# Kernel tuning notes

Measured on AMD Instinct MI355X. Metric: run time of the kernel, lower is better.

Reference implementation:

```python
import jax, jax.numpy as jnp
import numpy as np

BS, N, D, H = 4, 2048, 512, 8
DK = D // H
XAVIER_STD = float(np.sqrt(2.0 / (D + D)))  # xavier_normal_, gain=1


def setup_inputs() -> dict:
    key = jax.random.key(0)
    ks = jax.random.split(key, 10)
    Q = jax.random.normal(ks[0], (BS, N, D), jnp.float32)
    K = jax.random.normal(ks[1], (BS, N, D), jnp.float32)
    V = jax.random.normal(ks[2], (BS, N, D), jnp.float32)
    q_mas = jax.random.randint(ks[3], (BS, N, 1), 0, 2).astype(jnp.float32)
    k_mas = jax.random.randint(ks[4], (BS, N, 1), 0, 2).astype(jnp.float32)
    # 0/1 attention mask; force self-edges so no row is fully masked (avoids NaN softmax)
    att_mas = jax.random.randint(ks[5], (BS, N, N), 0, 2).astype(jnp.float32)
    att_mas = jnp.maximum(att_mas, jnp.eye(N, dtype=jnp.float32)[None])
    WQ = jax.random.normal(ks[6], (D, D), jnp.float32) * XAVIER_STD
    WK = jax.random.normal(ks[7], (D, D), jnp.float32) * XAVIER_STD
    WV = jax.random.normal(ks[8], (D, D), jnp.float32) * XAVIER_STD
    WO = jax.random.normal(ks[9], (D, D), jnp.float32) * XAVIER_STD
    return {"Q": Q, "K": K, "V": V, "q_mas": q_mas, "k_mas": k_mas,
            "att_mas": att_mas, "WQ": WQ, "WK": WK, "WV": WV, "WO": WO}


def reference(Q, K, V, q_mas, k_mas, att_mas, WQ, WK, WV, WO):
    bs, n, d = Q.shape
    h, dk = H, DK
    qm = q_mas.reshape(bs, 1, n, 1)  # (bs,1,n,1)
    km = k_mas.reshape(bs, 1, n, 1)
    # nn.Linear (no bias): x @ W.T ; split heads -> (bs,h,n,dk); apply pre-masks
    Qh = qm * (Q @ WQ.T).reshape(bs, n, h, dk).transpose(0, 2, 1, 3)
    Kh = km * (K @ WK.T).reshape(bs, n, h, dk).transpose(0, 2, 1, 3)
    Vh = km * (V @ WV.T).reshape(bs, n, h, dk).transpose(0, 2, 1, 3)
    scores = jnp.einsum('bhqd,bhkd->bhqk', Qh, Kh) / jnp.sqrt(jnp.float32(dk))
    mas = att_mas.reshape(bs, 1, n, n)
    scores = jnp.where(mas.astype(bool), scores, -jnp.inf)
    attn = jax.nn.softmax(scores, axis=-1) * mas
    y = jnp.einsum('bhqk,bhkd->bhqd', attn, Vh) * km  # post-mask (note: km over query dim, as in source)
    y = y.transpose(0, 2, 1, 3).reshape(bs, n, d)
    y = (y @ WO.T) * k_mas.reshape(bs, n, 1)
    return y
```

## Files before the change

kernel.cpp:

```cpp
#include <hip/hip_runtime.h>


#define BS_    4
#define NSEQ   2048
#define DMODEL 512
#define NH     8
#define DKH    64
#define MROWS  (BS_ * NSEQ)
#define NW32   (NSEQ / 32)
#define NWORDS (BS_ * NSEQ * NSEQ / 32)

typedef unsigned short ushort_t;
typedef __attribute__((ext_vector_type(8))) short short8;
typedef __attribute__((ext_vector_type(4))) float floatx4;

__device__ __forceinline__ ushort_t f2bf(float f) {
    unsigned int x = __builtin_bit_cast(unsigned int, f);
    unsigned int lsb = (x >> 16) & 1u;
    x += 0x7fffu + lsb;
    return (ushort_t)(x >> 16);
}
__device__ __forceinline__ floatx4 mfma_bf16(short8 a, short8 b, floatx4 c) {
    return __builtin_amdgcn_mfma_f32_16x16x32_bf16(a, b, c, 0, 0, 0);
}
__device__ __forceinline__ void gld16(const ushort_t* g, ushort_t* l) {
    __builtin_amdgcn_global_load_lds(
        (const __attribute__((address_space(1))) unsigned int*)g,
        (__attribute__((address_space(3))) unsigned int*)l, 16, 0, 0);
}
__device__ __forceinline__ unsigned int cvt_pk_bf16(float lo, float hi) {
    unsigned int r;
    asm("v_cvt_pk_bf16_f32 %0, %1, %2" : "=v"(r) : "v"(lo), "v"(hi));
    return r;
}

__global__ __launch_bounds__(256) void cvt_all(const float* __restrict__ a,
                                               const float* __restrict__ b,
                                               const float* __restrict__ c,
                                               const float* __restrict__ wq,
                                               const float* __restrict__ wk,
                                               const float* __restrict__ wv,
                                               const float* __restrict__ wo,
                                               const float* __restrict__ am,
                                               ushort_t* __restrict__ dst,
                                               ushort_t* __restrict__ wdst,
                                               unsigned int* __restrict__ mb, int n4) {
    const int i = blockIdx.x * blockDim.x + threadIdx.x;
    const int yy = blockIdx.y;
    if (yy == 4) {
        if (i < NWORDS) {
            const float4* src = (const float4*)am + (size_t)i * 8;
            unsigned int m = 0;
#pragma unroll
            for (int j = 0; j < 8; ++j) {
                const float4 v = src[j];
                m |= (v.x != 0.f ? 1u : 0u) << (4 * j);
                m |= (v.y != 0.f ? 1u : 0u) << (4 * j + 1);
                m |= (v.z != 0.f ? 1u : 0u) << (4 * j + 2);
                m |= (v.w != 0.f ? 1u : 0u) << (4 * j + 3);
            }
            mb[i] = m;
        }
        return;
    }
    if (yy == 3) {
        const int wn4 = DMODEL * DMODEL / 4;
        if (i < 4 * wn4) {
            const int w = i >> 16;
            const float* src = (w == 0) ? wq : (w == 1) ? wk : (w == 2) ? wv : wo;
            const float4 v = ((const float4*)src)[i & (wn4 - 1)];
            ushort4 o;
            o.x = f2bf(v.x); o.y = f2bf(v.y); o.z = f2bf(v.z); o.w = f2bf(v.w);
            ((ushort4*)wdst)[i] = o;
        }
        return;
    }
    const float* src = (yy == 0) ? a : (yy == 1) ? b : c;
    ushort_t* d = dst + (size_t)yy * ((size_t)n4 * 4);
    const float4 v = ((const float4*)src)[i];
    ushort4 o;
    o.x = f2bf(v.x); o.y = f2bf(v.y); o.z = f2bf(v.z); o.w = f2bf(v.w);
    ((ushort4*)d)[i] = o;
}

__global__ __launch_bounds__(256) void gemm_proj(const ushort_t* __restrict__ Xall,
                                                 const ushort_t* __restrict__ Wall,
                                                 const float* __restrict__ qmas,
                                                 const float* __restrict__ kmas,
                                                 ushort_t* __restrict__ Qh,
                                                 ushort_t* __restrict__ Kh,
                                                 ushort_t* __restrict__ Vt) {
    __shared__ ushort_t As[128 * 32];
    __shared__ ushort_t Bs[128 * 32];
    const int z = blockIdx.z;
    const ushort_t* X  = Xall + (size_t)z * MROWS * DMODEL;
    const ushort_t* Wb = Wall + (size_t)z * DMODEL * DMODEL;
    const float* rowmask = (z == 0) ? qmas : kmas;

    const int tid  = threadIdx.x;
    const int wave = tid >> 6;
    const int lane = tid & 63;
    const int l16  = lane & 15;
    const int quad = lane >> 4;
    const int wr   = wave >> 1;
    const int wc   = wave & 1;
    const int m0   = blockIdx.x * 128;
    const int n0   = blockIdx.y * 128;
    const int crow = lane >> 2;
    const int koff = (lane & 3) * 8;

    floatx4 acc[4][4];
#pragma unroll
    for (int t = 0; t < 4; ++t)
#pragma unroll
        for (int u = 0; u < 4; ++u) acc[t][u] = (floatx4){0.f, 0.f, 0.f, 0.f};

    for (int k0 = 0; k0 < DMODEL; k0 += 32) {
#pragma unroll
        for (int c2 = 0; c2 < 2; ++c2) {
            const int c = wave * 2 + c2;
            gld16(X  + (size_t)(m0 + c * 16 + crow) * DMODEL + k0 + koff, &As[c * 512]);
            gld16(Wb + (size_t)(n0 + c * 16 + crow) * DMODEL + k0 + koff, &Bs[c * 512]);
        }
        __syncthreads();
        short8 a[4], b[4];
#pragma unroll
        for (int t = 0; t < 4; ++t)
            a[t] = *(const short8*)&As[(wr * 64 + t * 16 + l16) * 32 + quad * 8];
#pragma unroll
        for (int u = 0; u < 4; ++u)
            b[u] = *(const short8*)&Bs[(wc * 64 + u * 16 + l16) * 32 + quad * 8];
#pragma unroll
        for (int t = 0; t < 4; ++t)
#pragma unroll
            for (int u = 0; u < 4; ++u) acc[t][u] = mfma_bf16(a[t], b[u], acc[t][u]);
        __syncthreads();
    }

    float rm[4][4];
#pragma unroll
    for (int t = 0; t < 4; ++t)
#pragma unroll
        for (int r = 0; r < 4; ++r)
            rm[t][r] = rowmask[m0 + wr * 64 + t * 16 + quad * 4 + r];
    if (z == 0) {
#pragma unroll
        for (int t = 0; t < 4; ++t)
#pragma unroll
            for (int r = 0; r < 4; ++r) rm[t][r] *= 0.18033688011112042f;
    }

    const int bb    = m0 >> 11;
    const int nbase = (m0 & (NSEQ - 1)) + wr * 64;
#pragma unroll
    for (int t = 0; t < 4; ++t) {
#pragma unroll
        for (int u = 0; u < 4; ++u) {
            const int d = n0 + wc * 64 + u * 16 + l16;
            const int h = d >> 6, cc = d & 63;
            if (z < 2) {
                ushort_t* dst = (z == 0) ? Qh : Kh;
#pragma unroll
                for (int r = 0; r < 4; ++r) {
                    const int n = nbase + t * 16 + quad * 4 + r;
                    dst[((size_t)(bb * NH + h) * NSEQ + n) * DKH + cc] =
                        f2bf(acc[t][u][r] * rm[t][r]);
                }
            } else {
                ushort4 pk;
                pk.x = f2bf(acc[t][u][0] * rm[t][0]);
                pk.y = f2bf(acc[t][u][1] * rm[t][1]);
                pk.z = f2bf(acc[t][u][2] * rm[t][2]);
                pk.w = f2bf(acc[t][u][3] * rm[t][3]);
                const int n = nbase + t * 16 + quad * 4;
                *(ushort4*)(Vt + ((size_t)(bb * NH + h) * DKH + cc) * NSEQ + n) = pk;
            }
        }
    }
}

__global__ __launch_bounds__(256) void gemm_out(const ushort_t* __restrict__ X,
                                                const ushort_t* __restrict__ Wb,
                                                const float* __restrict__ rowmask,
                                                float* __restrict__ dst) {
    __shared__ ushort_t As[128 * 32];
    __shared__ ushort_t Bs[128 * 32];
    const int tid  = threadIdx.x;
    const int wave = tid >> 6;
    const int lane = tid & 63;
    const int l16  = lane & 15;
    const int quad = lane >> 4;
    const int wr   = wave >> 1;
    const int wc   = wave & 1;
    const int m0   = blockIdx.x * 128;
    const int n0   = blockIdx.y * 128;
    const int crow = lane >> 2;
    const int koff = (lane & 3) * 8;

    floatx4 acc[4][4];
#pragma unroll
    for (int t = 0; t < 4; ++t)
#pragma unroll
        for (int u = 0; u < 4; ++u) acc[t][u] = (floatx4){0.f, 0.f, 0.f, 0.f};

    for (int k0 = 0; k0 < DMODEL; k0 += 32) {
#pragma unroll
        for (int c2 = 0; c2 < 2; ++c2) {
            const int c = wave * 2 + c2;
            gld16(X  + (size_t)(m0 + c * 16 + crow) * DMODEL + k0 + koff, &As[c * 512]);
            gld16(Wb + (size_t)(n0 + c * 16 + crow) * DMODEL + k0 + koff, &Bs[c * 512]);
        }
        __syncthreads();
        short8 a[4], b[4];
#pragma unroll
        for (int t = 0; t < 4; ++t)
            a[t] = *(const short8*)&As[(wr * 64 + t * 16 + l16) * 32 + quad * 8];
#pragma unroll
        for (int u = 0; u < 4; ++u)
            b[u] = *(const short8*)&Bs[(wc * 64 + u * 16 + l16) * 32 + quad * 8];
#pragma unroll
        for (int t = 0; t < 4; ++t)
#pragma unroll
            for (int u = 0; u < 4; ++u) acc[t][u] = mfma_bf16(a[t], b[u], acc[t][u]);
        __syncthreads();
    }

#pragma unroll
    for (int t = 0; t < 4; ++t) {
#pragma unroll
        for (int r = 0; r < 4; ++r) {
            const int m = m0 + wr * 64 + t * 16 + quad * 4 + r;
            const float rm = rowmask[m];
#pragma unroll
            for (int u = 0; u < 4; ++u) {
                const int d = n0 + wc * 64 + u * 16 + l16;
                dst[(size_t)m * DMODEL + d] = acc[t][u][r] * rm;
            }
        }
    }
}

__global__ __launch_bounds__(256) void attn_kernel(const ushort_t* __restrict__ Qh,
                                                   const ushort_t* __restrict__ Kh,
                                                   const ushort_t* __restrict__ Vt,
                                                   const unsigned int* __restrict__ Mb,
                                                   const float* __restrict__ kmas,
                                                   ushort_t* __restrict__ y) {
    __shared__ __align__(16) ushort_t Ks[128 * 72];
    __shared__ __align__(16) ushort_t Vs[64 * 136];
    __shared__ __align__(16) ushort_t Ps[4][16 * 136];

    const int tid  = threadIdx.x;
    const int wave = tid >> 6;
    const int lane = tid & 63;
    const int l16  = lane & 15;
    const int quad = lane >> 4;
    const int h    = blockIdx.y;
    const int b    = blockIdx.z;
    const int qw   = blockIdx.x * 64 + wave * 16;

    ushort_t* Psw = Ps[wave];

    const ushort_t* Kb = Kh + (size_t)(b * NH + h) * NSEQ * DKH;
    const ushort_t* Vb = Vt + (size_t)(b * NH + h) * DKH * NSEQ;
    const uint4* Mv = (const uint4*)(Mb + ((size_t)(b * NSEQ + qw) + l16) * NW32);

    const ushort_t* Qp = Qh + ((size_t)((b * NH + h) * NSEQ) + qw + l16) * DKH + quad * 8;
    const short8 qfa = *(const short8*)Qp;
    const short8 qfb = *(const short8*)(Qp + 32);

    float lpart = 0.f;
    floatx4 accO[4];
#pragma unroll
    for (int ct = 0; ct < 4; ++ct) accO[ct] = (floatx4){0.f, 0.f, 0.f, 0.f};

    short8 kv[4], vv[4];
    uint4 mwn;
#pragma unroll
    for (int i = 0; i < 4; ++i) {
        const int c = tid + i * 256;
        kv[i] = *(const short8*)(Kb + (size_t)(c >> 3) * DKH + (c & 7) * 8);
    }
#pragma unroll
    for (int i = 0; i < 4; ++i) {
        const int c = tid + i * 256;
        vv[i] = *(const short8*)(Vb + (size_t)(c >> 4) * NSEQ + (c & 15) * 8);
    }
    mwn = Mv[0];

    for (int kt = 0; kt < NSEQ / 128; ++kt) {
        const uint4 mw = mwn;

        __syncthreads();
#pragma unroll
        for (int i = 0; i < 4; ++i) {
            const int c = tid + i * 256;
            *(short8*)&Ks[(c >> 3) * 72 + (c & 7) * 8] = kv[i];
        }
#pragma unroll
        for (int i = 0; i < 4; ++i) {
            const int c = tid + i * 256;
            *(short8*)&Vs[(c >> 4) * 136 + (c & 15) * 8] = vv[i];
        }
        __syncthreads();

        if (kt + 1 < NSEQ / 128) {
            const int kn = (kt + 1) * 128;
#pragma unroll
            for (int i = 0; i < 4; ++i) {
                const int c = tid + i * 256;
                kv[i] = *(const short8*)(Kb + (size_t)(kn + (c >> 3)) * DKH + (c & 7) * 8);
            }
#pragma unroll
            for (int i = 0; i < 4; ++i) {
                const int c = tid + i * 256;
                vv[i] = *(const short8*)(Vb + (size_t)(c >> 4) * NSEQ + kn + (c & 15) * 8);
            }
            mwn = Mv[kt + 1];
        }

        const unsigned int wsh[4] = {mw.x >> (quad * 4), mw.y >> (quad * 4),
                                     mw.z >> (quad * 4), mw.w >> (quad * 4)};
#pragma unroll
        for (int fr = 0; fr < 8; ++fr) {
            const short8 ka = *(const short8*)&Ks[(fr * 16 + l16) * 72 + quad * 8];
            const short8 kb = *(const short8*)&Ks[(fr * 16 + l16) * 72 + 32 + quad * 8];
            floatx4 s = {0.f, 0.f, 0.f, 0.f};
            s = mfma_bf16(ka, qfa, s);
            s = mfma_bf16(kb, qfb, s);
            float p[4];
#pragma unroll
            for (int r = 0; r < 4; ++r) {
                const int bitp = ((fr & 1) << 4) + r;
                const unsigned int mm =
                    (unsigned int)__builtin_amdgcn_sbfe((int)wsh[fr >> 1], bitp, 1);
                const float e = exp2f(s[r]);
                const unsigned int pb = __builtin_bit_cast(unsigned int, e) & mm;
                p[r] = __builtin_bit_cast(float, pb);
                lpart += p[r];
            }
            uint2 pk;
            pk.x = cvt_pk_bf16(p[0], p[1]);
            pk.y = cvt_pk_bf16(p[2], p[3]);
            *(uint2*)&Psw[l16 * 136 + fr * 16 + quad * 4] = pk;
        }

        __builtin_amdgcn_wave_barrier();
        short8 pf[4];
#pragma unroll
        for (int kf = 0; kf < 4; ++kf)
            pf[kf] = *(const short8*)&Psw[l16 * 136 + kf * 32 + quad * 8];
        __builtin_amdgcn_wave_barrier();

#pragma unroll
        for (int ct = 0; ct < 4; ++ct) {
#pragma unroll
            for (int kf = 0; kf < 4; ++kf) {
                const short8 vb = *(const short8*)&Vs[(ct * 16 + l16) * 136 + kf * 32 + quad * 8];
                accO[ct] = mfma_bf16(pf[kf], vb, accO[ct]);
            }
        }
    }

    float lfull = lpart;
    lfull += __shfl_xor(lfull, 16);
    lfull += __shfl_xor(lfull, 32);
#pragma unroll
    for (int r = 0; r < 4; ++r) {
        const int q = qw + quad * 4 + r;
        const float l = __shfl(lfull, quad * 4 + r);
        const float scale = kmas[b * NSEQ + q] / l;
#pragma unroll
        for (int ct = 0; ct < 4; ++ct) {
            y[(size_t)(b * NSEQ + q) * DMODEL + h * DKH + ct * 16 + l16] =
                f2bf(accO[ct][r] * scale);
        }
    }
}

extern "C" void kernel_launch(void* const* d_in, const int* in_sizes, int n_in,
                              void* d_out, int out_size, void* d_ws, size_t ws_size,
                              hipStream_t stream) {
    (void)in_sizes; (void)n_in; (void)out_size; (void)ws_size;
    const float* Q  = (const float*)d_in[0];
    const float* K  = (const float*)d_in[1];
    const float* V  = (const float*)d_in[2];
    const float* qm = (const float*)d_in[3];
    const float* km = (const float*)d_in[4];
    const float* am = (const float*)d_in[5];
    const float* WQ = (const float*)d_in[6];
    const float* WK = (const float*)d_in[7];
    const float* WV = (const float*)d_in[8];
    const float* WO = (const float*)d_in[9];

    const size_t XN = (size_t)MROWS * DMODEL;
    const size_t WN = (size_t)DMODEL * DMODEL;
    ushort_t* Xbf = (ushort_t*)d_ws;
    ushort_t* Wbf = Xbf + 3 * XN;
    ushort_t* WOb = Wbf + 3 * WN;
    ushort_t* Qh  = Wbf + 4 * WN;
    ushort_t* Kh  = Qh + XN;
    ushort_t* Vt  = Kh + XN;
    ushort_t* y   = Vt + XN;
    unsigned int* Mbits = (unsigned int*)d_out;
    float* out = (float*)d_out;

    hipLaunchKernelGGL(cvt_all, dim3(4096, 5), dim3(256), 0, stream,
                       Q, K, V, WQ, WK, WV, WO, am, Xbf, Wbf, Mbits, (int)(XN / 4));

    hipLaunchKernelGGL(gemm_proj, dim3(MROWS / 128, DMODEL / 128, 3), dim3(256), 0, stream,
                       Xbf, Wbf, qm, km, Qh, Kh, Vt);

    hipLaunchKernelGGL(attn_kernel, dim3(NSEQ / 64, NH, BS_), dim3(256), 0, stream,
                       Qh, Kh, Vt, Mbits, km, y);

    hipLaunchKernelGGL(gemm_out, dim3(MROWS / 128, DMODEL / 128), dim3(256), 0, stream,
                       y, WOb, km, out);
}
```

Before: 291.0 us.

## Process two query tiles per wave in attention to reuse K/V tiles

Each wave now handles 32 query rows (two 16-row MFMA tiles) instead of 16, so each block covers 128 queries and the grid is halved. Every K and V tile loaded into shared memory is reused across twice as many queries, halving K/V global and LDS traffic per query. The register prefetch of the next K/V tile is removed, so global loads are issued in the same iteration they are consumed. This raises register and LDS use (the P buffers double) and may reduce occupancy and overlap.

```diff
diff --git a/kernel.cpp b/kernel.cpp
--- a/kernel.cpp
+++ b/kernel.cpp
@@ -248,7 +248,7 @@
                                                    ushort_t* __restrict__ y) {
     __shared__ __align__(16) ushort_t Ks[128 * 72];
     __shared__ __align__(16) ushort_t Vs[64 * 136];
-    __shared__ __align__(16) ushort_t Ps[4][16 * 136];
+    __shared__ __align__(16) ushort_t Ps[8][16 * 136];
 
     const int tid  = threadIdx.x;
     const int wave = tid >> 6;
@@ -257,39 +257,47 @@
     const int quad = lane >> 4;
     const int h    = blockIdx.y;
     const int b    = blockIdx.z;
-    const int qw   = blockIdx.x * 64 + wave * 16;
-
-    ushort_t* Psw = Ps[wave];
+    const int qw   = blockIdx.x * 128 + wave * 32;
+
+    ushort_t* Ps0 = Ps[wave * 2];
+    ushort_t* Ps1 = Ps[wave * 2 + 1];
 
     const ushort_t* Kb = Kh + (size_t)(b * NH + h) * NSEQ * DKH;
     const ushort_t* Vb = Vt + (size_t)(b * NH + h) * DKH * NSEQ;
-    const uint4* Mv = (const uint4*)(Mb + ((size_t)(b * NSEQ + qw) + l16) * NW32);
-
-    const ushort_t* Qp = Qh + ((size_t)((b * NH + h) * NSEQ) + qw + l16) * DKH + quad * 8;
-    const short8 qfa = *(const short8*)Qp;
-    const short8 qfb = *(const short8*)(Qp + 32);
-
-    float lpart = 0.f;
-    floatx4 accO[4];
-#pragma unroll
-    for (int ct = 0; ct < 4; ++ct) accO[ct] = (floatx4){0.f, 0.f, 0.f, 0.f};
-
-    short8 kv[4], vv[4];
-    uint4 mwn;
-#pragma unroll
-    for (int i = 0; i < 4; ++i) {
-        const int c = tid + i * 256;
-        kv[i] = *(const short8*)(Kb + (size_t)(c >> 3) * DKH + (c & 7) * 8);
-    }
-#pragma unroll
-    for (int i = 0; i < 4; ++i) {
-        const int c = tid + i * 256;
-        vv[i] = *(const short8*)(Vb + (size_t)(c >> 4) * NSEQ + (c & 15) * 8);
-    }
-    mwn = Mv[0];
+    const uint4* Mv0 = (const uint4*)(Mb + ((size_t)(b * NSEQ + qw) + l16) * NW32);
+    const uint4* Mv1 = (const uint4*)(Mb + ((size_t)(b * NSEQ + qw) + 16 + l16) * NW32);
+
+    const ushort_t* Qp0 = Qh + ((size_t)((b * NH + h) * NSEQ) + qw + l16) * DKH + quad * 8;
+    const ushort_t* Qp1 = Qp0 + 16 * DKH;
+    const short8 qf0a = *(const short8*)Qp0;
+    const short8 qf0b = *(const short8*)(Qp0 + 32);
+    const short8 qf1a = *(const short8*)Qp1;
+    const short8 qf1b = *(const short8*)(Qp1 + 32);
+
+    float lp0 = 0.f, lp1 = 0.f;
+    floatx4 accA[4], accB[4];
+#pragma unroll
+    for (int ct = 0; ct < 4; ++ct) {
+        accA[ct] = (floatx4){0.f, 0.f, 0.f, 0.f};
+        accB[ct] = (floatx4){0.f, 0.f, 0.f, 0.f};
+    }
 
     for (int kt = 0; kt < NSEQ / 128; ++kt) {
-        const uint4 mw = mwn;
+        const int k0 = kt * 128;
+
+        short8 kv[4], vv[4];
+#pragma unroll
+        for (int i = 0; i < 4; ++i) {
+            const int c = tid + i * 256;
+            kv[i] = *(const short8*)(Kb + (size_t)(k0 + (c >> 3)) * DKH + (c & 7) * 8);
+        }
+#pragma unroll
+        for (int i = 0; i < 4; ++i) {
+            const int c = tid + i * 256;
+            vv[i] = *(const short8*)(Vb + (size_t)(c >> 4) * NSEQ + k0 + (c & 15) * 8);
+        }
+        const uint4 mw0 = Mv0[kt];
+        const uint4 mw1 = Mv1[kt];
 
         __syncthreads();
 #pragma unroll
@@ -304,52 +312,54 @@
         }
         __syncthreads();
 
-        if (kt + 1 < NSEQ / 128) {
-            const int kn = (kt + 1) * 128;
-#pragma unroll
-            for (int i = 0; i < 4; ++i) {
-                const int c = tid + i * 256;
-                kv[i] = *(const short8*)(Kb + (size_t)(kn + (c >> 3)) * DKH + (c & 7) * 8);
-            }
-#pragma unroll
-            for (int i = 0; i < 4; ++i) {
-                const int c = tid + i * 256;
-                vv[i] = *(const short8*)(Vb + (size_t)(c >> 4) * NSEQ + kn + (c & 15) * 8);
-            }
-            mwn = Mv[kt + 1];
-        }
-
-        const unsigned int wsh[4] = {mw.x >> (quad * 4), mw.y >> (quad * 4),
-                                     mw.z >> (quad * 4), mw.w >> (quad * 4)};
+        const unsigned int wsh0[4] = {mw0.x >> (quad * 4), mw0.y >> (quad * 4),
+                                      mw0.z >> (quad * 4), mw0.w >> (quad * 4)};
+        const unsigned int wsh1[4] = {mw1.x >> (quad * 4), mw1.y >> (quad * 4),
+                                      mw1.z >> (quad * 4), mw1.w >> (quad * 4)};
 #pragma unroll
         for (int fr = 0; fr < 8; ++fr) {
             const short8 ka = *(const short8*)&Ks[(fr * 16 + l16) * 72 + quad * 8];
             const short8 kb = *(const short8*)&Ks[(fr * 16 + l16) * 72 + 32 + quad * 8];
-            floatx4 s = {0.f, 0.f, 0.f, 0.f};
-            s = mfma_bf16(ka, qfa, s);
-            s = mfma_bf16(kb, qfb, s);
-            float p[4];
+            floatx4 s0 = {0.f, 0.f, 0.f, 0.f};
+            s0 = mfma_bf16(ka, qf0a, s0);
+            s0 = mfma_bf16(kb, qf0b, s0);
+            floatx4 s1 = {0.f, 0.f, 0.f, 0.f};
+            s1 = mfma_bf16(ka, qf1a, s1);
+            s1 = mfma_bf16(kb, qf1b, s1);
+
+            float p0[4], p1[4];
 #pragma unroll
             for (int r = 0; r < 4; ++r) {
                 const int bitp = ((fr & 1) << 4) + r;
-                const unsigned int mm =
-                    (unsigned int)__builtin_amdgcn_sbfe((int)wsh[fr >> 1], bitp, 1);
-                const float e = exp2f(s[r]);
-                const unsigned int pb = __builtin_bit_cast(unsigned int, e) & mm;
-                p[r] = __builtin_bit_cast(float, pb);
-                lpart += p[r];
+                const unsigned int m0m =
+                    (unsigned int)__builtin_amdgcn_sbfe((int)wsh0[fr >> 1], bitp, 1);
+                const unsigned int m1m =
+                    (unsigned int)__builtin_amdgcn_sbfe((int)wsh1[fr >> 1], bitp, 1);
+                const unsigned int pb0 =
+                    __builtin_bit_cast(unsigned int, exp2f(s0[r])) & m0m;
+                const unsigned int pb1 =
+                    __builtin_bit_cast(unsigned int, exp2f(s1[r])) & m1m;
+                p0[r] = __builtin_bit_cast(float, pb0);
+                p1[r] = __builtin_bit_cast(float, pb1);
+                lp0 += p0[r];
+                lp1 += p1[r];
             }
-            uint2 pk;
-            pk.x = cvt_pk_bf16(p[0], p[1]);
-            pk.y = cvt_pk_bf16(p[2], p[3]);
-            *(uint2*)&Psw[l16 * 136 + fr * 16 + quad * 4] = pk;
+            uint2 pk0, pk1;
+            pk0.x = cvt_pk_bf16(p0[0], p0[1]);
+            pk0.y = cvt_pk_bf16(p0[2], p0[3]);
+            pk1.x = cvt_pk_bf16(p1[0], p1[1]);
+            pk1.y = cvt_pk_bf16(p1[2], p1[3]);
+            *(uint2*)&Ps0[l16 * 136 + fr * 16 + quad * 4] = pk0;
+            *(uint2*)&Ps1[l16 * 136 + fr * 16 + quad * 4] = pk1;
         }
 
         __builtin_amdgcn_wave_barrier();
-        short8 pf[4];
-#pragma unroll
-        for (int kf = 0; kf < 4; ++kf)
-            pf[kf] = *(const short8*)&Psw[l16 * 136 + kf * 32 + quad * 8];
+        short8 pf0[4], pf1[4];
+#pragma unroll
+        for (int kf = 0; kf < 4; ++kf) {
+            pf0[kf] = *(const short8*)&Ps0[l16 * 136 + kf * 32 + quad * 8];
+            pf1[kf] = *(const short8*)&Ps1[l16 * 136 + kf * 32 + quad * 8];
+        }
         __builtin_amdgcn_wave_barrier();
 
 #pragma unroll
@@ -357,23 +367,31 @@
 #pragma unroll
             for (int kf = 0; kf < 4; ++kf) {
                 const short8 vb = *(const short8*)&Vs[(ct * 16 + l16) * 136 + kf * 32 + quad * 8];
-                accO[ct] = mfma_bf16(pf[kf], vb, accO[ct]);
+                accA[ct] = mfma_bf16(pf0[kf], vb, accA[ct]);
+                accB[ct] = mfma_bf16(pf1[kf], vb, accB[ct]);
             }
         }
     }
 
-    float lfull = lpart;
-    lfull += __shfl_xor(lfull, 16);
-    lfull += __shfl_xor(lfull, 32);
+    float lf0 = lp0, lf1 = lp1;
+    lf0 += __shfl_xor(lf0, 16);
+    lf0 += __shfl_xor(lf0, 32);
+    lf1 += __shfl_xor(lf1, 16);
+    lf1 += __shfl_xor(lf1, 32);
 #pragma unroll
     for (int r = 0; r < 4; ++r) {
-        const int q = qw + quad * 4 + r;
-        const float l = __shfl(lfull, quad * 4 + r);
-        const float scale = kmas[b * NSEQ + q] / l;
+        const int q0 = qw + quad * 4 + r;
+        const int q1 = q0 + 16;
+        const float l0 = __shfl(lf0, quad * 4 + r);
+        const float l1 = __shfl(lf1, quad * 4 + r);
+        const float sc0 = kmas[b * NSEQ + q0] / l0;
+        const float sc1 = kmas[b * NSEQ + q1] / l1;
 #pragma unroll
         for (int ct = 0; ct < 4; ++ct) {
-            y[(size_t)(b * NSEQ + q) * DMODEL + h * DKH + ct * 16 + l16] =
-                f2bf(accO[ct][r] * scale);
+            y[(size_t)(b * NSEQ + q0) * DMODEL + h * DKH + ct * 16 + l16] =
+                f2bf(accA[ct][r] * sc0);
+            y[(size_t)(b * NSEQ + q1) * DMODEL + h * DKH + ct * 16 + l16] =
+                f2bf(accB[ct][r] * sc1);
         }
     }
 }
@@ -411,7 +429,7 @@
     hipLaunchKernelGGL(gemm_proj, dim3(MROWS / 128, DMODEL / 128, 3), dim3(256), 0, stream,
                        Xbf, Wbf, qm, km, Qh, Kh, Vt);
 
-    hipLaunchKernelGGL(attn_kernel, dim3(NSEQ / 64, NH, BS_), dim3(256), 0, stream,
+    hipLaunchKernelGGL(attn_kernel, dim3(NSEQ / 128, NH, BS_), dim3(256), 0, stream,
                        Qh, Kh, Vt, Mbits, km, y);
 
     hipLaunchKernelGGL(gemm_out, dim3(MROWS / 128, DMODEL / 128), dim3(256), 0, stream,
```

Measured after the change: 281.9 us. -3.1%, faster.
